# Kernel tuning notes

Hardware: AMD Instinct MI355X
Metric: run time of the kernel (lower is better)

## Reference

```python
import jax, jax.numpy as jnp
import numpy as np

B, L, C, H = 4, 4096, 1024, 16


def setup_inputs() -> dict:
    key = jax.random.key(0)
    k1, k2, k3 = jax.random.split(key, 3)
    x = jax.random.normal(k1, (B, L, C), dtype=jnp.float32)
    # torch nn.Linear params: weight (out, in), bias (out,)
    W_qkv = jax.random.normal(k2, (3 * C, C), dtype=jnp.float32) * 0.02
    b_qkv = jnp.zeros((3 * C,), dtype=jnp.float32)
    W_out = jax.random.normal(k3, (C, C), dtype=jnp.float32) * 0.02
    b_out = jnp.zeros((C,), dtype=jnp.float32)
    return {"x": x, "W_qkv": W_qkv, "b_qkv": b_qkv, "W_out": W_out,
            "b_out": b_out, "num_heads": H}


def reference(x, W_qkv, b_qkv, W_out, b_out, num_heads):
    # Faithful to the source, INCLUDING its head-axis bug:
    # q,k,v stay (B, L, H, D); attention is computed over the HEAD axis
    # (H x H per token), and the final transpose(1,2).reshape scrambles
    # sequence/head layout exactly as torch does.
    b, l, c = x.shape
    h = num_heads
    d = c // h
    scale = d ** (-0.5)
    qkv = (x @ W_qkv.T + b_qkv).reshape(b, l, 3, h, d)
    q, k, v = qkv[:, :, 0], qkv[:, :, 1], qkv[:, :, 2]  # (B, L, H, D)
    # (B,L,H,D) @ (B,L,D,H) -> (B,L,H,H)
    attn = jnp.einsum('blhd,blgd->blhg', q, k) * scale
    attn = jax.nn.softmax(attn, axis=-1)
    # dropout is identity in eval mode
    out = jnp.einsum('blhg,blgd->blhd', attn, v)      # (B, L, H, D)
    out = jnp.swapaxes(out, 1, 2).reshape(b, l, c)    # torch transpose(1,2).reshape
    return out @ W_out.T + b_out
```

## Files before the change

kernel.cpp:

```cpp
#include <hip/hip_runtime.h>
#include <hip/hip_bf16.h>


typedef __attribute__((ext_vector_type(8))) short bf16x8;
typedef __attribute__((ext_vector_type(4))) float f32x4;

__device__ __forceinline__ float bf2f(unsigned short u) {
    union { unsigned int i; float f; } x;
    x.i = ((unsigned int)u) << 16;
    return x.f;
}
__device__ __forceinline__ unsigned short f2bf(float f) {
    unsigned int u = __float_as_uint(f);
    u = (u + 0x7FFFu + ((u >> 16) & 1u)) >> 16;
    return (unsigned short)u;
}

#define VMCNT4() asm volatile("s_waitcnt vmcnt(4)" ::: "memory")
#define VMCNT0() asm volatile("s_waitcnt vmcnt(0)" ::: "memory")
#define BAR()    __builtin_amdgcn_s_barrier()
#define SCHED0() __builtin_amdgcn_sched_barrier(0)

__global__ __launch_bounds__(256) void cast_all(const float* __restrict__ x,
                                                const float* __restrict__ wq,
                                                const float* __restrict__ wo,
                                                unsigned short* __restrict__ xb,
                                                unsigned short* __restrict__ wqb,
                                                unsigned short* __restrict__ wob) {
    const size_t base = (size_t)blockIdx.x * 2048 + threadIdx.x;
#pragma unroll
    for (int it = 0; it < 8; ++it) {
        size_t i = base + (size_t)it * 256;
        const float4* s; ushort4* d; size_t off;
        if (i < 4194304)      { s = (const float4*)x;  d = (ushort4*)xb;  off = i; }
        else if (i < 4980736) { s = (const float4*)wq; d = (ushort4*)wqb; off = i - 4194304; }
        else                  { s = (const float4*)wo; d = (ushort4*)wob; off = i - 4980736; }
        float4 v = s[off];
        ushort4 o;
        o.x = f2bf(v.x); o.y = f2bf(v.y); o.z = f2bf(v.z); o.w = f2bf(v.w);
        d[off] = o;
    }
}

template<int OUTF32>
__global__ __launch_bounds__(512, 2) void gemm256(const unsigned short* __restrict__ A,
                                                  const unsigned short* __restrict__ B,
                                                  const float* __restrict__ bias,
                                                  unsigned short* __restrict__ Cb,
                                                  float* __restrict__ Cf,
                                                  int M, int N, int K, int NXT) {
    __shared__ __align__(16) unsigned short lds[2][2][2][8192];

    const int tid  = threadIdx.x;
    const int lane = tid & 63;
    const int wave = tid >> 6;
    const int wr = wave >> 2;
    const int wc = wave & 3;
    const int fr = lane & 15;
    const int fq = lane >> 4;
    const int frx = fr & 7;

    const int nwg  = gridDim.x;
    const int orig = blockIdx.x;
    const int wg   = (orig & 7) * (nwg >> 3) + (orig >> 3);
    const int tileM = (wg / NXT) * 256;
    const int tileN = (wg % NXT) * 256;

    const int r8  = tid >> 3;
    const int jsw = (tid & 7) ^ (r8 & 7);
    const unsigned short* Ap = A;
    const unsigned short* Bp = B;

#define STAGE(nb, OPp, HH, ktt) do {                                                   \
    const unsigned short* gb = (OPp) ? Bp : Ap;                                        \
    const int rb = ((OPp) ? tileN : tileM) + (HH) * 128 + r8;                          \
    const unsigned short* s0 = gb + (size_t)rb * K + (ktt) * 64 + jsw * 8;             \
    unsigned short* d0 = &lds[nb][OPp][HH][tid * 8];                                   \
    __builtin_amdgcn_global_load_lds((const __attribute__((address_space(1))) void*)s0,\
        (__attribute__((address_space(3))) void*)d0, 16, 0, 0);                        \
    __builtin_amdgcn_global_load_lds(                                                  \
        (const __attribute__((address_space(1))) void*)(s0 + (size_t)64 * K),          \
        (__attribute__((address_space(3))) void*)(d0 + 4096), 16, 0, 0);               \
} while (0)

#define READ_A(bb, h) do {                                                             \
    _Pragma("unroll") for (int i2 = 0; i2 < 4; ++i2) {                                 \
        const int ar = (wr * 64 + i2 * 16 + fr) * 64;                                  \
        af[i2][0] = *(const bf16x8*)&lds[bb][0][h][ar + ((fq ^ frx) << 3)];            \
        af[i2][1] = *(const bf16x8*)&lds[bb][0][h][ar + (((4 + fq) ^ frx) << 3)];      \
    }                                                                                  \
} while (0)

#define READ_B(bb, g) do {                                                             \
    _Pragma("unroll") for (int j2 = 0; j2 < 2; ++j2) {                                 \
        const int br = (wc * 32 + j2 * 16 + fr) * 64;                                  \
        bfr[2*(g)+j2][0] = *(const bf16x8*)&lds[bb][1][g][br + ((fq ^ frx) << 3)];     \
        bfr[2*(g)+j2][1] = *(const bf16x8*)&lds[bb][1][g][br + (((4 + fq) ^ frx) << 3)];\
    }                                                                                  \
} while (0)

#define MFMA_Q(h, g) do {                                                              \
    __builtin_amdgcn_s_setprio(1);                                                     \
    _Pragma("unroll") for (int i2 = 0; i2 < 4; ++i2)                                   \
    _Pragma("unroll") for (int j2 = 0; j2 < 2; ++j2) {                                 \
        acc[(h)*4+i2][(g)*2+j2] = __builtin_amdgcn_mfma_f32_16x16x32_bf16(             \
            af[i2][0], bfr[2*(g)+j2][0], acc[(h)*4+i2][(g)*2+j2], 0, 0, 0);            \
        acc[(h)*4+i2][(g)*2+j2] = __builtin_amdgcn_mfma_f32_16x16x32_bf16(             \
            af[i2][1], bfr[2*(g)+j2][1], acc[(h)*4+i2][(g)*2+j2], 0, 0, 0);            \
    }                                                                                  \
    __builtin_amdgcn_s_setprio(0);                                                     \
} while (0)

    f32x4 acc[8][4];
#pragma unroll
    for (int i = 0; i < 8; ++i)
#pragma unroll
        for (int j = 0; j < 4; ++j) acc[i][j] = (f32x4){0.f, 0.f, 0.f, 0.f};

    STAGE(0, 0, 0, 0);
    STAGE(0, 1, 0, 0);
    STAGE(0, 1, 1, 0);
    STAGE(0, 0, 1, 0);

    const int NT = K >> 6;
    int cur = 0;
    for (int kt = 0; kt < NT - 1; ++kt) {
        const int nb = cur ^ 1;
        BAR();
        STAGE(nb, 0, 0, kt + 1);
        STAGE(nb, 1, 0, kt + 1);
        VMCNT4();
        BAR();
        SCHED0();
        bf16x8 af[4][2], bfr[4][2];
        READ_A(cur, 0); READ_B(cur, 0); READ_B(cur, 1);
        MFMA_Q(0, 0);
        STAGE(nb, 1, 1, kt + 1);
        STAGE(nb, 0, 1, kt + 1);
        MFMA_Q(0, 1);
        READ_A(cur, 1);
        MFMA_Q(1, 0);
        MFMA_Q(1, 1);
        cur = nb;
    }
    BAR();
    VMCNT0();
    BAR();
    SCHED0();
    {
        bf16x8 af[4][2], bfr[4][2];
        READ_A(cur, 0); READ_B(cur, 0); READ_B(cur, 1);
        MFMA_Q(0, 0);
        MFMA_Q(0, 1);
        READ_A(cur, 1);
        MFMA_Q(1, 0);
        MFMA_Q(1, 1);
    }

#pragma unroll
    for (int i = 0; i < 8; ++i) {
        const int row = tileM + (i >> 2) * 128 + wr * 64 + (i & 3) * 16 + fq * 4;
#pragma unroll
        for (int j = 0; j < 4; ++j) {
            const int col = tileN + (j >> 1) * 128 + wc * 32 + (j & 1) * 16 + fr;
            const float bv = bias[col];
#pragma unroll
            for (int r = 0; r < 4; ++r) {
                const float v = acc[i][j][r] + bv;
                if (OUTF32) Cf[(size_t)(row + r) * N + col] = v;
                else        Cb[(size_t)(row + r) * N + col] = f2bf(v);
            }
        }
    }
#undef STAGE
#undef READ_A
#undef READ_B
#undef MFMA_Q
}

__global__ __launch_bounds__(256) void attn_kernel(const unsigned short* __restrict__ qkv,
                                                   unsigned short* __restrict__ scr) {
    __shared__ __align__(16) unsigned short sbuf[4][3328];
    __shared__ float Pl[4][256];

    const int wave = threadIdx.x >> 6, lane = threadIdx.x & 63;
    const int token = blockIdx.x * 4 + wave;
    const int b = token >> 12, l = token & 4095;

    const unsigned short* src = qkv + (size_t)token * 3072;
    unsigned short* sw = sbuf[wave];
#pragma unroll
    for (int i = 0; i < 2; ++i) {
        const int c = lane + i * 64;
        const int row = c >> 3, j8 = (c & 7) * 8;
        *(bf16x8*)&sw[row * 72 + j8]        = *(const bf16x8*)&src[c * 8];
        *(bf16x8*)&sw[1152 + row * 72 + j8] = *(const bf16x8*)&src[1024 + c * 8];
        *(bf16x8*)&sw[2304 + c * 8]         = *(const bf16x8*)&src[2048 + c * 8];
    }
    __syncthreads();

    float sv[4];
#pragma unroll
    for (int r = 0; r < 4; ++r) {
        const int p = r * 64 + lane;
        const int h = p >> 4, g = p & 15;
        float acc = 0.f;
#pragma unroll
        for (int d8 = 0; d8 < 8; ++d8) {
            bf16x8 qa = *(const bf16x8*)&sw[h * 72 + d8 * 8];
            bf16x8 kb = *(const bf16x8*)&sw[1152 + g * 72 + d8 * 8];
#pragma unroll
            for (int j = 0; j < 8; ++j)
                acc += bf2f((unsigned short)qa[j]) * bf2f((unsigned short)kb[j]);
        }
        sv[r] = acc * 0.125f;
    }

#pragma unroll
    for (int r = 0; r < 4; ++r) {
        float m = sv[r];
        m = fmaxf(m, __shfl_xor(m, 1));
        m = fmaxf(m, __shfl_xor(m, 2));
        m = fmaxf(m, __shfl_xor(m, 4));
        m = fmaxf(m, __shfl_xor(m, 8));
        float e = __expf(sv[r] - m);
        float s = e;
        s += __shfl_xor(s, 1);
        s += __shfl_xor(s, 2);
        s += __shfl_xor(s, 4);
        s += __shfl_xor(s, 8);
        Pl[wave][r * 64 + lane] = e / s;
    }
    __syncthreads();

    float vreg[16];
#pragma unroll
    for (int g = 0; g < 16; ++g) vreg[g] = bf2f(sw[2304 + g * 64 + lane]);

    const int q_ = l >> 4, j = l & 15;
    const size_t base = ((size_t)b * 4096 + q_) * 1024 + j * 64 + lane;
#pragma unroll
    for (int h = 0; h < 16; ++h) {
        float acc = 0.f;
#pragma unroll
        for (int g = 0; g < 16; ++g) acc += Pl[wave][h * 16 + g] * vreg[g];
        scr[base + (size_t)h * 256 * 1024] = f2bf(acc);
    }
}

extern "C" void kernel_launch(void* const* d_in, const int* in_sizes, int n_in,
                              void* d_out, int out_size, void* d_ws, size_t ws_size,
                              hipStream_t stream) {
    const float* x    = (const float*)d_in[0];
    const float* Wqkv = (const float*)d_in[1];
    const float* bqkv = (const float*)d_in[2];
    const float* Wout = (const float*)d_in[3];
    const float* bout = (const float*)d_in[4];
    float* out = (float*)d_out;

    char* ws = (char*)d_ws;
    unsigned short* xb   = (unsigned short*)(ws);
    unsigned short* wqb  = (unsigned short*)(ws + 33554432);
    unsigned short* wob  = (unsigned short*)(ws + 39845888);
    unsigned short* qkvb = (unsigned short*)(ws + 41943040);
    unsigned short* scr  = (unsigned short*)(ws + 142606336);

    cast_all<<<2560, 256, 0, stream>>>(x, Wqkv, Wout, xb, wqb, wob);

    gemm256<0><<<768, 512, 0, stream>>>(xb, wqb, bqkv, qkvb, nullptr, 16384, 3072, 1024, 12);

    attn_kernel<<<4096, 256, 0, stream>>>(qkvb, scr);

    gemm256<1><<<256, 512, 0, stream>>>(scr, wob, bout, nullptr, out, 16384, 1024, 1024, 4);
}
```

Before: 196.0 us.

## Switch GEMM inner loop from 16x16x32 to 32x32x16 bf16 MFMA

Replaces the 16x16x32 MFMA tiling in the 256x256 GEMM with 32x32x16 MFMA instructions. The fragment loading, loop schedule and epilogue row/column mapping are reworked to match. Each wave now issues fewer, larger MFMAs and reads fewer LDS fragments per k-step, aiming for higher matrix-core throughput. The trade-offs are a different interleaving of LDS reads with global staging, and an epilogue store pattern whose coalescing may change.

After: 206.2 us. 1.05x slower.

```diff
diff --git a/kernel.cpp b/kernel.cpp
--- a/kernel.cpp
+++ b/kernel.cpp
@@ -2,8 +2,9 @@
 #include <hip/hip_bf16.h>
 
 
-typedef __attribute__((ext_vector_type(8))) short bf16x8;
-typedef __attribute__((ext_vector_type(4))) float f32x4;
+typedef __attribute__((ext_vector_type(8)))  short bf16x8;
+typedef __attribute__((ext_vector_type(4)))  float f32x4;
+typedef __attribute__((ext_vector_type(16))) float f32x16;
 
 __device__ __forceinline__ float bf2f(unsigned short u) {
     union { unsigned int i; float f; } x;
@@ -56,9 +57,8 @@
     const int wave = tid >> 6;
     const int wr = wave >> 2;
     const int wc = wave & 3;
-    const int fr = lane & 15;
-    const int fq = lane >> 4;
-    const int frx = fr & 7;
+    const int l31 = lane & 31;
+    const int kc  = lane >> 5;
 
     const int nwg  = gridDim.x;
     const int orig = blockIdx.x;
@@ -83,39 +83,35 @@
         (__attribute__((address_space(3))) void*)(d0 + 4096), 16, 0, 0);               \
 } while (0)
 
-#define READ_A(bb, h) do {                                                             \
-    _Pragma("unroll") for (int i2 = 0; i2 < 4; ++i2) {                                 \
-        const int ar = (wr * 64 + i2 * 16 + fr) * 64;                                  \
-        af[i2][0] = *(const bf16x8*)&lds[bb][0][h][ar + ((fq ^ frx) << 3)];            \
-        af[i2][1] = *(const bf16x8*)&lds[bb][0][h][ar + (((4 + fq) ^ frx) << 3)];      \
+#define READ_K(bb, kk) do {                                                            \
+    _Pragma("unroll") for (int m = 0; m < 4; ++m) {                                    \
+        const int rl = wr * 64 + (m & 1) * 32 + l31;                                   \
+        const int c  = (kk) * 2 + kc;                                                  \
+        afk[m] = *(const bf16x8*)&lds[bb][0][m >> 1][rl * 64 + ((c ^ (rl & 7)) << 3)]; \
+    }                                                                                  \
+    _Pragma("unroll") for (int n = 0; n < 2; ++n) {                                    \
+        const int cl = wc * 32 + l31;                                                  \
+        const int c  = (kk) * 2 + kc;                                                  \
+        bfk[n] = *(const bf16x8*)&lds[bb][1][n][cl * 64 + ((c ^ (cl & 7)) << 3)];      \
     }                                                                                  \
 } while (0)
 
-#define READ_B(bb, g) do {                                                             \
-    _Pragma("unroll") for (int j2 = 0; j2 < 2; ++j2) {                                 \
-        const int br = (wc * 32 + j2 * 16 + fr) * 64;                                  \
-        bfr[2*(g)+j2][0] = *(const bf16x8*)&lds[bb][1][g][br + ((fq ^ frx) << 3)];     \
-        bfr[2*(g)+j2][1] = *(const bf16x8*)&lds[bb][1][g][br + (((4 + fq) ^ frx) << 3)];\
-    }                                                                                  \
-} while (0)
-
-#define MFMA_Q(h, g) do {                                                              \
+#define MFMA_K() do {                                                                  \
     __builtin_amdgcn_s_setprio(1);                                                     \
-    _Pragma("unroll") for (int i2 = 0; i2 < 4; ++i2)                                   \
-    _Pragma("unroll") for (int j2 = 0; j2 < 2; ++j2) {                                 \
-        acc[(h)*4+i2][(g)*2+j2] = __builtin_amdgcn_mfma_f32_16x16x32_bf16(             \
-            af[i2][0], bfr[2*(g)+j2][0], acc[(h)*4+i2][(g)*2+j2], 0, 0, 0);            \
-        acc[(h)*4+i2][(g)*2+j2] = __builtin_amdgcn_mfma_f32_16x16x32_bf16(             \
-            af[i2][1], bfr[2*(g)+j2][1], acc[(h)*4+i2][(g)*2+j2], 0, 0, 0);            \
-    }                                                                                  \
+    _Pragma("unroll") for (int m = 0; m < 4; ++m)                                      \
+    _Pragma("unroll") for (int n = 0; n < 2; ++n)                                      \
+        acc[m][n] = __builtin_amdgcn_mfma_f32_32x32x16_bf16(afk[m], bfk[n],            \
+                                                            acc[m][n], 0, 0, 0);       \
     __builtin_amdgcn_s_setprio(0);                                                     \
 } while (0)
 
-    f32x4 acc[8][4];
-#pragma unroll
-    for (int i = 0; i < 8; ++i)
-#pragma unroll
-        for (int j = 0; j < 4; ++j) acc[i][j] = (f32x4){0.f, 0.f, 0.f, 0.f};
+    f32x16 acc[4][2];
+#pragma unroll
+    for (int m = 0; m < 4; ++m)
+#pragma unroll
+        for (int n = 0; n < 2; ++n)
+#pragma unroll
+            for (int r = 0; r < 16; ++r) acc[m][n][r] = 0.f;
 
     STAGE(0, 0, 0, 0);
     STAGE(0, 1, 0, 0);
@@ -132,15 +128,13 @@
         VMCNT4();
         BAR();
         SCHED0();
-        bf16x8 af[4][2], bfr[4][2];
-        READ_A(cur, 0); READ_B(cur, 0); READ_B(cur, 1);
-        MFMA_Q(0, 0);
+        bf16x8 afk[4], bfk[2];
+        READ_K(cur, 0); MFMA_K();
         STAGE(nb, 1, 1, kt + 1);
         STAGE(nb, 0, 1, kt + 1);
-        MFMA_Q(0, 1);
-        READ_A(cur, 1);
-        MFMA_Q(1, 0);
-        MFMA_Q(1, 1);
+        READ_K(cur, 1); MFMA_K();
+        READ_K(cur, 2); MFMA_K();
+        READ_K(cur, 3); MFMA_K();
         cur = nb;
     }
     BAR();
@@ -148,34 +142,32 @@
     BAR();
     SCHED0();
     {
-        bf16x8 af[4][2], bfr[4][2];
-        READ_A(cur, 0); READ_B(cur, 0); READ_B(cur, 1);
-        MFMA_Q(0, 0);
-        MFMA_Q(0, 1);
-        READ_A(cur, 1);
-        MFMA_Q(1, 0);
-        MFMA_Q(1, 1);
-    }
-
-#pragma unroll
-    for (int i = 0; i < 8; ++i) {
-        const int row = tileM + (i >> 2) * 128 + wr * 64 + (i & 3) * 16 + fq * 4;
-#pragma unroll
-        for (int j = 0; j < 4; ++j) {
-            const int col = tileN + (j >> 1) * 128 + wc * 32 + (j & 1) * 16 + fr;
-            const float bv = bias[col];
-#pragma unroll
-            for (int r = 0; r < 4; ++r) {
-                const float v = acc[i][j][r] + bv;
-                if (OUTF32) Cf[(size_t)(row + r) * N + col] = v;
-                else        Cb[(size_t)(row + r) * N + col] = f2bf(v);
+        bf16x8 afk[4], bfk[2];
+        READ_K(cur, 0); MFMA_K();
+        READ_K(cur, 1); MFMA_K();
+        READ_K(cur, 2); MFMA_K();
+        READ_K(cur, 3); MFMA_K();
+    }
+
+#pragma unroll
+    for (int n = 0; n < 2; ++n) {
+        const int col = tileN + n * 128 + wc * 32 + l31;
+        const float bv = bias[col];
+#pragma unroll
+        for (int m = 0; m < 4; ++m) {
+            const int rbase = tileM + (m >> 1) * 128 + wr * 64 + (m & 1) * 32 + 4 * kc;
+#pragma unroll
+            for (int r = 0; r < 16; ++r) {
+                const int row = rbase + (r & 3) + 8 * (r >> 2);
+                const float v = acc[m][n][r] + bv;
+                if (OUTF32) Cf[(size_t)row * N + col] = v;
+                else        Cb[(size_t)row * N + col] = f2bf(v);
             }
         }
     }
 #undef STAGE
-#undef READ_A
-#undef READ_B
-#undef MFMA_Q
+#undef READ_K
+#undef MFMA_K
 }
 
 __global__ __launch_bounds__(256) void attn_kernel(const unsigned short* __restrict__ qkv,
```

## Split GEMM tile across 16 waves with 64x64 per-wave subtiles

Applied to the files above, without the earlier changes.

The GEMM block grows from 512 to 1024 threads, and each wave now computes a 64x64 output subtile instead of a 128x128 quadrant set. Staging issues one global-to-LDS load per thread per half-tile, and the wait count is adjusted to match. This lowers accumulator register pressure per wave and raises the number of waves per CU. In exchange, each wave reuses fewer fragments, so LDS read traffic per MFMA goes up.

After: 198.9 us. No clear change (+1.5%).

```diff
diff --git a/kernel.cpp b/kernel.cpp
--- a/kernel.cpp
+++ b/kernel.cpp
@@ -16,7 +16,7 @@
     return (unsigned short)u;
 }
 
-#define VMCNT4() asm volatile("s_waitcnt vmcnt(4)" ::: "memory")
+#define VMCNT2() asm volatile("s_waitcnt vmcnt(2)" ::: "memory")
 #define VMCNT0() asm volatile("s_waitcnt vmcnt(0)" ::: "memory")
 #define BAR()    __builtin_amdgcn_s_barrier()
 #define SCHED0() __builtin_amdgcn_sched_barrier(0)
@@ -43,12 +43,12 @@
 }
 
 template<int OUTF32>
-__global__ __launch_bounds__(512, 2) void gemm256(const unsigned short* __restrict__ A,
-                                                  const unsigned short* __restrict__ B,
-                                                  const float* __restrict__ bias,
-                                                  unsigned short* __restrict__ Cb,
-                                                  float* __restrict__ Cf,
-                                                  int M, int N, int K, int NXT) {
+__global__ __launch_bounds__(1024, 1) void gemm256(const unsigned short* __restrict__ A,
+                                                   const unsigned short* __restrict__ B,
+                                                   const float* __restrict__ bias,
+                                                   unsigned short* __restrict__ Cb,
+                                                   float* __restrict__ Cf,
+                                                   int M, int N, int K, int NXT) {
     __shared__ __align__(16) unsigned short lds[2][2][2][8192];
 
     const int tid  = threadIdx.x;
@@ -58,7 +58,8 @@
     const int wc = wave & 3;
     const int fr = lane & 15;
     const int fq = lane >> 4;
-    const int frx = fr & 7;
+    const int ha = wr >> 1;
+    const int hb = wc >> 1;
 
     const int nwg  = gridDim.x;
     const int orig = blockIdx.x;
@@ -78,42 +79,31 @@
     unsigned short* d0 = &lds[nb][OPp][HH][tid * 8];                                   \
     __builtin_amdgcn_global_load_lds((const __attribute__((address_space(1))) void*)s0,\
         (__attribute__((address_space(3))) void*)d0, 16, 0, 0);                        \
-    __builtin_amdgcn_global_load_lds(                                                  \
-        (const __attribute__((address_space(1))) void*)(s0 + (size_t)64 * K),          \
-        (__attribute__((address_space(3))) void*)(d0 + 4096), 16, 0, 0);               \
 } while (0)
 
-#define READ_A(bb, h) do {                                                             \
+#define READ_K(bb, ks) do {                                                            \
     _Pragma("unroll") for (int i2 = 0; i2 < 4; ++i2) {                                 \
-        const int ar = (wr * 64 + i2 * 16 + fr) * 64;                                  \
-        af[i2][0] = *(const bf16x8*)&lds[bb][0][h][ar + ((fq ^ frx) << 3)];            \
-        af[i2][1] = *(const bf16x8*)&lds[bb][0][h][ar + (((4 + fq) ^ frx) << 3)];      \
+        const int lr = (wr & 1) * 64 + i2 * 16 + fr;                                   \
+        af[i2] = *(const bf16x8*)&lds[bb][0][ha][lr * 64 + ((((ks)*4+fq) ^ (lr & 7)) << 3)];\
+    }                                                                                  \
+    _Pragma("unroll") for (int j2 = 0; j2 < 4; ++j2) {                                 \
+        const int lc = (wc & 1) * 64 + j2 * 16 + fr;                                   \
+        bf[j2] = *(const bf16x8*)&lds[bb][1][hb][lc * 64 + ((((ks)*4+fq) ^ (lc & 7)) << 3)];\
     }                                                                                  \
 } while (0)
 
-#define READ_B(bb, g) do {                                                             \
-    _Pragma("unroll") for (int j2 = 0; j2 < 2; ++j2) {                                 \
-        const int br = (wc * 32 + j2 * 16 + fr) * 64;                                  \
-        bfr[2*(g)+j2][0] = *(const bf16x8*)&lds[bb][1][g][br + ((fq ^ frx) << 3)];     \
-        bfr[2*(g)+j2][1] = *(const bf16x8*)&lds[bb][1][g][br + (((4 + fq) ^ frx) << 3)];\
-    }                                                                                  \
-} while (0)
-
-#define MFMA_Q(h, g) do {                                                              \
+#define MFMA_K() do {                                                                  \
     __builtin_amdgcn_s_setprio(1);                                                     \
     _Pragma("unroll") for (int i2 = 0; i2 < 4; ++i2)                                   \
-    _Pragma("unroll") for (int j2 = 0; j2 < 2; ++j2) {                                 \
-        acc[(h)*4+i2][(g)*2+j2] = __builtin_amdgcn_mfma_f32_16x16x32_bf16(             \
-            af[i2][0], bfr[2*(g)+j2][0], acc[(h)*4+i2][(g)*2+j2], 0, 0, 0);            \
-        acc[(h)*4+i2][(g)*2+j2] = __builtin_amdgcn_mfma_f32_16x16x32_bf16(             \
-            af[i2][1], bfr[2*(g)+j2][1], acc[(h)*4+i2][(g)*2+j2], 0, 0, 0);            \
-    }                                                                                  \
+    _Pragma("unroll") for (int j2 = 0; j2 < 4; ++j2)                                   \
+        acc[i2][j2] = __builtin_amdgcn_mfma_f32_16x16x32_bf16(af[i2], bf[j2],          \
+                                                              acc[i2][j2], 0, 0, 0);   \
     __builtin_amdgcn_s_setprio(0);                                                     \
 } while (0)
 
-    f32x4 acc[8][4];
-#pragma unroll
-    for (int i = 0; i < 8; ++i)
+    f32x4 acc[4][4];
+#pragma unroll
+    for (int i = 0; i < 4; ++i)
 #pragma unroll
         for (int j = 0; j < 4; ++j) acc[i][j] = (f32x4){0.f, 0.f, 0.f, 0.f};
 
@@ -129,18 +119,14 @@
         BAR();
         STAGE(nb, 0, 0, kt + 1);
         STAGE(nb, 1, 0, kt + 1);
-        VMCNT4();
+        VMCNT2();
         BAR();
         SCHED0();
-        bf16x8 af[4][2], bfr[4][2];
-        READ_A(cur, 0); READ_B(cur, 0); READ_B(cur, 1);
-        MFMA_Q(0, 0);
+        bf16x8 af[4], bf[4];
+        READ_K(cur, 0); MFMA_K();
         STAGE(nb, 1, 1, kt + 1);
         STAGE(nb, 0, 1, kt + 1);
-        MFMA_Q(0, 1);
-        READ_A(cur, 1);
-        MFMA_Q(1, 0);
-        MFMA_Q(1, 1);
+        READ_K(cur, 1); MFMA_K();
         cur = nb;
     }
     BAR();
@@ -148,21 +134,17 @@
     BAR();
     SCHED0();
     {
-        bf16x8 af[4][2], bfr[4][2];
-        READ_A(cur, 0); READ_B(cur, 0); READ_B(cur, 1);
-        MFMA_Q(0, 0);
-        MFMA_Q(0, 1);
-        READ_A(cur, 1);
-        MFMA_Q(1, 0);
-        MFMA_Q(1, 1);
-    }
-
-#pragma unroll
-    for (int i = 0; i < 8; ++i) {
-        const int row = tileM + (i >> 2) * 128 + wr * 64 + (i & 3) * 16 + fq * 4;
+        bf16x8 af[4], bf[4];
+        READ_K(cur, 0); MFMA_K();
+        READ_K(cur, 1); MFMA_K();
+    }
+
+#pragma unroll
+    for (int i = 0; i < 4; ++i) {
+        const int row = tileM + wr * 64 + i * 16 + fq * 4;
 #pragma unroll
         for (int j = 0; j < 4; ++j) {
-            const int col = tileN + (j >> 1) * 128 + wc * 32 + (j & 1) * 16 + fr;
+            const int col = tileN + wc * 64 + j * 16 + fr;
             const float bv = bias[col];
 #pragma unroll
             for (int r = 0; r < 4; ++r) {
@@ -173,9 +155,8 @@
         }
     }
 #undef STAGE
-#undef READ_A
-#undef READ_B
-#undef MFMA_Q
+#undef READ_K
+#undef MFMA_K
 }
 
 __global__ __launch_bounds__(256) void attn_kernel(const unsigned short* __restrict__ qkv,
@@ -267,9 +248,9 @@
 
     cast_all<<<2560, 256, 0, stream>>>(x, Wqkv, Wout, xb, wqb, wob);
 
-    gemm256<0><<<768, 512, 0, stream>>>(xb, wqb, bqkv, qkvb, nullptr, 16384, 3072, 1024, 12);
+    gemm256<0><<<768, 1024, 0, stream>>>(xb, wqb, bqkv, qkvb, nullptr, 16384, 3072, 1024, 12);
 
     attn_kernel<<<4096, 256, 0, stream>>>(qkvb, scr);
 
-    gemm256<1><<<256, 512, 0, stream>>>(scr, wob, bout, nullptr, out, 16384, 1024, 1024, 4);
-}
+    gemm256<1><<<256, 1024, 0, stream>>>(scr, wob, bout, nullptr, out, 16384, 1024, 1024, 4);
+}
```
